# Performance work log

Measured on AMD Instinct MI355X. Metric: run time of the kernel, lower is better.

Reference implementation:

```python
import jax, jax.numpy as jnp
import numpy as np

B, A, C, M, E = 8, 100000, 8, 128, 32
ALPHA, GAMMA = 0.25, 2.0


def setup_inputs() -> dict:
    key = jax.random.key(0)
    k1, k2, k3, k4, k5, k6, k7 = jax.random.split(key, 7)
    classifications = jax.random.uniform(k1, (B, A, C), dtype=jnp.float32)
    regressions = jax.random.normal(k2, (B, A, 8), dtype=jnp.float32)
    embeddings = jax.random.normal(k3, (B, A, E), dtype=jnp.float32)
    # anchors: random centers on a 1920x1080 image, reasonable w/h -> x1,y1,x2,y2
    cx = jax.random.uniform(k4, (A,), minval=0.0, maxval=1920.0)
    cy = jax.random.uniform(jax.random.fold_in(k4, 1), (A,), minval=0.0, maxval=1080.0)
    w = jax.random.uniform(jax.random.fold_in(k4, 2), (A,), minval=16.0, maxval=256.0)
    h = jax.random.uniform(jax.random.fold_in(k4, 3), (A,), minval=16.0, maxval=256.0)
    anchors = jnp.stack([cx - 0.5 * w, cy - 0.5 * h, cx + 0.5 * w, cy + 0.5 * h], axis=1)[None].astype(jnp.float32)
    # annotations: 16 coords = jittered 3D-box corner projections around a random box,
    # col 16 = object id, col 17 = class label in [0, C)
    bcx = jax.random.uniform(k5, (B, M, 1), minval=100.0, maxval=1820.0)
    bcy = jax.random.uniform(jax.random.fold_in(k5, 1), (B, M, 1), minval=100.0, maxval=980.0)
    bw = jax.random.uniform(jax.random.fold_in(k5, 2), (B, M, 1), minval=30.0, maxval=300.0)
    bh = jax.random.uniform(jax.random.fold_in(k5, 3), (B, M, 1), minval=30.0, maxval=300.0)
    jit = jax.random.uniform(k6, (B, M, 16), minval=-0.4, maxval=0.4)
    sx = jnp.array([-1, -1, 1, 1, -1, -1, 1, 1], jnp.float32)
    sy = jnp.array([-1, 1, -1, 1, -1, 1, -1, 1], jnp.float32)
    xs = bcx + 0.5 * bw * (sx + jit[..., 0:16:2])
    ys = bcy + 0.5 * bh * (sy + jit[..., 1:16:2])
    coords = jnp.stack([xs, ys], axis=-1).reshape(B, M, 16)
    ids = jax.random.randint(k7, (B, M, 1), 0, 1000).astype(jnp.float32)
    cls_lab = jax.random.randint(jax.random.fold_in(k7, 1), (B, M, 1), 0, C).astype(jnp.float32)
    annotations = jnp.concatenate([coords, ids, cls_lab], axis=-1)
    return {
        "classifications": classifications,
        "regressions": regressions,
        "anchors": anchors,
        "annotations": annotations,
        "embeddings": embeddings,
    }


def calc_iou(a, b):
    # a: [A,4], b: [M,4] in x1,y1,x2,y2 -> [A,M]
    area = (b[:, 2] - b[:, 0]) * (b[:, 3] - b[:, 1])
    iw = jnp.minimum(a[:, 2:3], b[None, :, 2]) - jnp.maximum(a[:, 0:1], b[None, :, 0])
    ih = jnp.minimum(a[:, 3:4], b[None, :, 3]) - jnp.maximum(a[:, 1:2], b[None, :, 1])
    iw = jnp.clip(iw, 0.0)
    ih = jnp.clip(ih, 0.0)
    ua = ((a[:, 2] - a[:, 0]) * (a[:, 3] - a[:, 1]))[:, None] + area[None, :] - iw * ih
    return iw * ih / jnp.clip(ua, 1e-8)


_S2 = jnp.array([-1, -1, 1, 1, -1, -1, 1, 1], jnp.float32)
_S4 = jnp.array([-1, 1, -1, 1, -1, 1, -1, 1], jnp.float32)
_S6 = jnp.array([1, 1, 1, 1, -1, -1, -1, -1], jnp.float32)


def _per_image(cls, reg, ann, anchor):
    # cls [A,C], reg [A,8], ann [M,18], anchor [A,4]
    aw = anchor[:, 2] - anchor[:, 0]
    ah = anchor[:, 3] - anchor[:, 1]
    acx = anchor[:, 0] + 0.5 * aw
    acy = anchor[:, 1] + 0.5 * ah
    cls = jnp.clip(cls, 1e-4, 1.0 - 1e-4)
    valid = ann[:, -1] >= 0.0  # [M]; annotations with class -1 are padding
    xs, ys = ann[:, 0:16:2], ann[:, 1:16:2]
    box2d = jnp.stack([xs.min(1), ys.min(1), xs.max(1), ys.max(1)], axis=1)  # [M,4]
    iou = jnp.where(valid[None, :], calc_iou(anchor, box2d), -1.0)  # [A,M]
    iou_max = iou.max(1)
    assigned = ann[iou.argmax(1)]  # [A,18]
    pos = iou_max >= 0.5
    neg = iou_max < 0.4
    num_pos = jnp.maximum(pos.sum().astype(cls.dtype), 1.0)

    onehot = jax.nn.one_hot(assigned[:, -1].astype(jnp.int32), cls.shape[1], dtype=cls.dtype)
    targets = jnp.where(pos[:, None], onehot, jnp.where(neg[:, None], 0.0, -1.0))
    alpha_f = jnp.where(targets == 1.0, ALPHA, 1.0 - ALPHA)
    focal_w = alpha_f * jnp.where(targets == 1.0, 1.0 - cls, cls) ** GAMMA
    bce = -(targets * jnp.log(cls) + (1.0 - targets) * jnp.log(1.0 - cls))
    cls_loss = jnp.where(targets != -1.0, focal_w * bce, 0.0).sum() / num_pos

    t = assigned[:, :16]

    def vp(rx, ry, tx, ty):
        denom = jnp.sqrt(rx * rx + ry * ry) * jnp.sqrt(tx * tx + ty * ty)
        return 1.0 - (rx * tx + ry * ty) / jnp.maximum(denom, 1e-8)

    vp1 = vp(reg[:, 2], reg[:, 3],
             (t[:, 4] + t[:, 6] + t[:, 12] + t[:, 14] - (t[:, 0] + t[:, 2] + t[:, 8] + t[:, 10])) / 4.0,
             (t[:, 5] + t[:, 7] + t[:, 13] + t[:, 15] - (t[:, 1] + t[:, 3] + t[:, 9] + t[:, 11])) / 4.0)
    vp2 = vp(reg[:, 4], reg[:, 5],
             (t[:, 2] + t[:, 6] + t[:, 10] + t[:, 14] - (t[:, 0] + t[:, 4] + t[:, 8] + t[:, 12])) / 4.0,
             (t[:, 3] + t[:, 7] + t[:, 11] + t[:, 15] - (t[:, 1] + t[:, 5] + t[:, 9] + t[:, 13])) / 4.0)
    vp3 = vp(reg[:, 6], reg[:, 7],
             (t[:, 0] + t[:, 2] + t[:, 4] + t[:, 6] - (t[:, 8] + t[:, 10] + t[:, 12] + t[:, 14])) / 4.0,
             (t[:, 1] + t[:, 3] + t[:, 5] + t[:, 7] - (t[:, 9] + t[:, 11] + t[:, 13] + t[:, 15])) / 4.0)
    vp_all = (vp1 + vp2 + vp3) / 3.0
    vp_loss = (vp_all * pos).sum() / num_pos

    # corner predictions from (ctr_x, ctr_y, v1, v2, v3) offsets: [A,8] x-coords, [A,8] y-coords
    px = reg[:, 0:1] + reg[:, 2:3] * _S2 + reg[:, 4:5] * _S4 + reg[:, 6:7] * _S6
    py = reg[:, 1:2] + reg[:, 3:4] * _S2 + reg[:, 5:6] * _S4 + reg[:, 7:8] * _S6
    tx = (t[:, 0:16:2] - acx[:, None]) / aw[:, None]
    ty = (t[:, 1:16:2] - acy[:, None]) / ah[:, None]
    diff = jnp.concatenate([jnp.abs(px - tx), jnp.abs(py - ty)], axis=1)  # [A,16]
    sl1 = jnp.where(diff <= 1.0 / 9.0, 0.5 * 9.0 * diff * diff, diff - 0.5 / 9.0)
    reg_loss = (sl1.mean(1) * pos).sum() / num_pos
    return cls_loss, reg_loss, vp_loss


def reference(classifications, regressions, anchors, annotations, embeddings):
    anchor = anchors[0]
    cls_l, reg_l, vp_l = jax.vmap(_per_image, in_axes=(0, 0, 0, None))(
        classifications, regressions, annotations, anchor)
    return jnp.stack([cls_l.mean(), reg_l.mean(), vp_l.mean()])


if __name__ == "__main__":
    print(reference(**setup_inputs()))
```

## Files before the change

### kernel.cpp

```cpp
#include <hip/hip_runtime.h>
#include <hip/hip_bf16.h>

namespace {

constexpr int B_N = 8;
constexpr int A_N = 100000;
constexpr int C_N = 8;
constexpr int M_N = 128;
constexpr int BLOCK = 256;
constexpr int NBLK = (A_N + BLOCK - 1) / BLOCK;

__global__ __launch_bounds__(BLOCK) void focal_main(
    const float* __restrict__ cls_,
    const float* __restrict__ reg_,
    const float* __restrict__ anchors_,
    const float* __restrict__ ann_,
    float* __restrict__ partials)
{
    __shared__ float  s_ann[M_N * 18];
    __shared__ float4 s_bb[M_N];
    __shared__ float4 s_meta[M_N];

    const int b   = blockIdx.y;
    const int tid = threadIdx.x;

    const float* annb = ann_ + (size_t)b * M_N * 18;
    for (int i = tid; i < M_N * 18; i += BLOCK) s_ann[i] = annb[i];
    __syncthreads();
    if (tid < M_N) {
        const float* t = s_ann + tid * 18;
        float minx = t[0], maxx = t[0], miny = t[1], maxy = t[1];
#pragma unroll
        for (int j = 1; j < 8; ++j) {
            minx = fminf(minx, t[2 * j]);     maxx = fmaxf(maxx, t[2 * j]);
            miny = fminf(miny, t[2 * j + 1]); maxy = fmaxf(maxy, t[2 * j + 1]);
        }
        s_bb[tid] = make_float4(minx, miny, maxx, maxy);
        const float area = (maxx - minx) * (maxy - miny);
        const float c    = t[17];
        s_meta[tid] = make_float4(area, c, (c >= 0.0f) ? 1.0f : 0.0f, 0.0f);
    }
    __syncthreads();

    const int a = blockIdx.x * BLOCK + tid;
    float clsS = 0.f, regS = 0.f, vpS = 0.f, posC = 0.f;

    if (a < A_N) {
        const float4 an   = ((const float4*)anchors_)[a];
        const float  aw   = an.z - an.x;
        const float  ah   = an.w - an.y;
        const float  acx  = an.x + 0.5f * aw;
        const float  acy  = an.y + 0.5f * ah;
        const float  aarea = aw * ah;

        float bn = -1.0f, bd = 1.0f;
        int   kbest = 0;
        for (int m = 0; m < M_N; ++m) {
            const float4 bb = s_bb[m];
            const float4 mt = s_meta[m];
            float iw = fminf(an.z, bb.z) - fmaxf(an.x, bb.x);
            float ih = fminf(an.w, bb.w) - fmaxf(an.y, bb.y);
            iw = fmaxf(iw, 0.0f);
            ih = fmaxf(ih, 0.0f);
            const float inter = iw * ih;
            const float ua    = fmaxf(aarea + mt.x - inter, 1e-8f);
            const bool  upd   = (mt.z > 0.0f) && (inter * bd > bn * ua);
            if (upd) { bn = inter; bd = ua; kbest = m; }
        }
        const float iou_max = (bn < 0.0f) ? -1.0f : bn / bd;
        const bool  pos = (iou_max >= 0.5f);
        const bool  neg = (iou_max <  0.4f);

        if (pos | neg) {
            const float* cp = cls_ + ((size_t)b * A_N + a) * C_N;
            const float4 c0 = ((const float4*)cp)[0];
            const float4 c1 = ((const float4*)cp)[1];
            const float pv[8] = {c0.x, c0.y, c0.z, c0.w, c1.x, c1.y, c1.z, c1.w};
            const int kc = pos ? (int)s_meta[kbest].y : -1;
            float sneg = 0.f, pkc = 0.5f, negkc = 0.f;
#pragma unroll
            for (int c = 0; c < C_N; ++c) {
                const float pc   = fminf(fmaxf(pv[c], 1e-4f), 1.0f - 1e-4f);
                const float term = 0.75f * pc * pc * (-__logf(1.0f - pc));
                sneg += term;
                if (c == kc) { pkc = pc; negkc = term; }
            }
            clsS = pos ? (sneg - negkc +
                          0.25f * (1.0f - pkc) * (1.0f - pkc) * (-__logf(pkc)))
                       : sneg;
        }

        if (pos) {
            posC = 1.0f;
            const float* rp = reg_ + ((size_t)b * A_N + a) * 8;
            const float4 r0 = ((const float4*)rp)[0];
            const float4 r1 = ((const float4*)rp)[1];
            const float* t  = s_ann + kbest * 18;
            float tt[16];
#pragma unroll
            for (int j = 0; j < 16; ++j) tt[j] = t[j];

            auto vp = [](float rx, float ry, float tx, float ty) {
                const float denom = sqrtf(rx * rx + ry * ry) * sqrtf(tx * tx + ty * ty);
                return 1.0f - (rx * tx + ry * ty) / fmaxf(denom, 1e-8f);
            };
            const float vp1 = vp(r0.z, r0.w,
                (tt[4] + tt[6] + tt[12] + tt[14] - (tt[0] + tt[2] + tt[8] + tt[10])) * 0.25f,
                (tt[5] + tt[7] + tt[13] + tt[15] - (tt[1] + tt[3] + tt[9] + tt[11])) * 0.25f);
            const float vp2 = vp(r1.x, r1.y,
                (tt[2] + tt[6] + tt[10] + tt[14] - (tt[0] + tt[4] + tt[8] + tt[12])) * 0.25f,
                (tt[3] + tt[7] + tt[11] + tt[15] - (tt[1] + tt[5] + tt[9] + tt[13])) * 0.25f);
            const float vp3 = vp(r1.z, r1.w,
                (tt[0] + tt[2] + tt[4] + tt[6] - (tt[8] + tt[10] + tt[12] + tt[14])) * 0.25f,
                (tt[1] + tt[3] + tt[5] + tt[7] - (tt[9] + tt[11] + tt[13] + tt[15])) * 0.25f);
            vpS = (vp1 + vp2 + vp3) * (1.0f / 3.0f);

            const float s2[8] = {-1, -1, 1, 1, -1, -1, 1, 1};
            const float s4[8] = {-1, 1, -1, 1, -1, 1, -1, 1};
            const float s6[8] = {1, 1, 1, 1, -1, -1, -1, -1};
            float ssum = 0.f;
#pragma unroll
            for (int j = 0; j < 8; ++j) {
                const float px = r0.x + r0.z * s2[j] + r1.x * s4[j] + r1.z * s6[j];
                const float py = r0.y + r0.w * s2[j] + r1.y * s4[j] + r1.w * s6[j];
                const float tx = (tt[2 * j]     - acx) / aw;
                const float ty = (tt[2 * j + 1] - acy) / ah;
                const float dx = fabsf(px - tx);
                const float dy = fabsf(py - ty);
                ssum += (dx <= (1.0f / 9.0f)) ? 4.5f * dx * dx : dx - (0.5f / 9.0f);
                ssum += (dy <= (1.0f / 9.0f)) ? 4.5f * dy * dy : dy - (0.5f / 9.0f);
            }
            regS = ssum * (1.0f / 16.0f);
        }
    }

#pragma unroll
    for (int off = 32; off; off >>= 1) {
        clsS += __shfl_down(clsS, off);
        regS += __shfl_down(regS, off);
        vpS  += __shfl_down(vpS, off);
        posC += __shfl_down(posC, off);
    }
    __shared__ float s_red[4][4];
    const int wv = tid >> 6, ln = tid & 63;
    if (ln == 0) {
        s_red[wv][0] = clsS; s_red[wv][1] = regS;
        s_red[wv][2] = vpS;  s_red[wv][3] = posC;
    }
    __syncthreads();
    if (tid == 0) {
        float C = 0, R = 0, V = 0, P = 0;
        for (int w = 0; w < 4; ++w) {
            C += s_red[w][0]; R += s_red[w][1];
            V += s_red[w][2]; P += s_red[w][3];
        }
        float* out = partials + ((size_t)b * NBLK + blockIdx.x) * 4;
        out[0] = C; out[1] = R; out[2] = V; out[3] = P;
    }
}

__global__ __launch_bounds__(BLOCK) void reduce_img(
    const float* __restrict__ partials,
    float* __restrict__ imgloss)
{
    const int b = blockIdx.x, tid = threadIdx.x;
    float c = 0.f, r = 0.f, v = 0.f, p = 0.f;
    for (int i = tid; i < NBLK; i += BLOCK) {
        const float* q = partials + ((size_t)b * NBLK + i) * 4;
        c += q[0]; r += q[1]; v += q[2]; p += q[3];
    }
#pragma unroll
    for (int off = 32; off; off >>= 1) {
        c += __shfl_down(c, off); r += __shfl_down(r, off);
        v += __shfl_down(v, off); p += __shfl_down(p, off);
    }
    __shared__ float s[4][4];
    const int wv = tid >> 6, ln = tid & 63;
    if (ln == 0) { s[wv][0] = c; s[wv][1] = r; s[wv][2] = v; s[wv][3] = p; }
    __syncthreads();
    if (tid == 0) {
        float C = 0, R = 0, V = 0, P = 0;
        for (int w = 0; w < 4; ++w) {
            C += s[w][0]; R += s[w][1]; V += s[w][2]; P += s[w][3];
        }
        const float np_ = fmaxf(P, 1.0f);
        imgloss[b * 3 + 0] = C / np_;
        imgloss[b * 3 + 1] = R / np_;
        imgloss[b * 3 + 2] = V / np_;
    }
}

__global__ void final_avg(const float* __restrict__ imgloss,
                          float* __restrict__ out)
{
    const int k = threadIdx.x;
    if (k < 3) {
        float s = 0.f;
        for (int b = 0; b < B_N; ++b) s += imgloss[b * 3 + k];
        out[k] = s * 0.125f;
    }
}

}

extern "C" void kernel_launch(void* const* d_in, const int* in_sizes, int n_in,
                              void* d_out, int out_size, void* d_ws, size_t ws_size,
                              hipStream_t stream)
{
    const float* cls_    = (const float*)d_in[0];
    const float* reg_    = (const float*)d_in[1];
    const float* anchors = (const float*)d_in[2];
    const float* ann     = (const float*)d_in[3];

    float* partials = (float*)d_ws;
    float* imgloss  = partials + (size_t)B_N * NBLK * 4;

    dim3 grid(NBLK, B_N);
    focal_main<<<grid, dim3(BLOCK), 0, stream>>>(cls_, reg_, anchors, ann, partials);
    reduce_img<<<dim3(B_N), dim3(BLOCK), 0, stream>>>(partials, imgloss);
    final_avg<<<dim3(1), dim3(64), 0, stream>>>(imgloss, (float*)d_out);
}
```

Before: 78.42 us.

## Process two anchors per thread and streamline the IoU argmax loop

```diff
diff --git a/kernel.cpp b/kernel.cpp
--- a/kernel.cpp
+++ b/kernel.cpp
@@ -8,7 +8,9 @@
 constexpr int C_N = 8;
 constexpr int M_N = 128;
 constexpr int BLOCK = 256;
-constexpr int NBLK = (A_N + BLOCK - 1) / BLOCK;
+constexpr int APT = 2;
+constexpr int TILE = BLOCK * APT;
+constexpr int NBLK = (A_N + TILE - 1) / TILE;
 
 __global__ __launch_bounds__(BLOCK) void focal_main(
     const float* __restrict__ cls_,
@@ -17,88 +19,114 @@
     const float* __restrict__ ann_,
     float* __restrict__ partials)
 {
-    __shared__ float  s_ann[M_N * 18];
     __shared__ float4 s_bb[M_N];
-    __shared__ float4 s_meta[M_N];
+    __shared__ float  s_area[M_N];
 
     const int b   = blockIdx.y;
     const int tid = threadIdx.x;
-
     const float* annb = ann_ + (size_t)b * M_N * 18;
-    for (int i = tid; i < M_N * 18; i += BLOCK) s_ann[i] = annb[i];
+
+    if (tid < M_N) {
+        const float* t = annb + tid * 18;
+        float minx = t[0], maxx = t[0], miny = t[1], maxy = t[1];
+#pragma unroll
+        for (int j = 1; j < 8; ++j) {
+            const float xj = t[2 * j], yj = t[2 * j + 1];
+            minx = fminf(minx, xj); maxx = fmaxf(maxx, xj);
+            miny = fminf(miny, yj); maxy = fmaxf(maxy, yj);
+        }
+        float area = (maxx - minx) * (maxy - miny);
+        if (t[17] < 0.0f) {
+            minx = INFINITY; miny = INFINITY; maxx = -INFINITY; maxy = -INFINITY;
+            area = 0.0f;
+        }
+        s_bb[tid]   = make_float4(minx, miny, maxx, maxy);
+        s_area[tid] = area;
+    }
     __syncthreads();
-    if (tid < M_N) {
-        const float* t = s_ann + tid * 18;
-        float minx = t[0], maxx = t[0], miny = t[1], maxy = t[1];
-#pragma unroll
-        for (int j = 1; j < 8; ++j) {
-            minx = fminf(minx, t[2 * j]);     maxx = fmaxf(maxx, t[2 * j]);
-            miny = fminf(miny, t[2 * j + 1]); maxy = fmaxf(maxy, t[2 * j + 1]);
-        }
-        s_bb[tid] = make_float4(minx, miny, maxx, maxy);
-        const float area = (maxx - minx) * (maxy - miny);
-        const float c    = t[17];
-        s_meta[tid] = make_float4(area, c, (c >= 0.0f) ? 1.0f : 0.0f, 0.0f);
-    }
-    __syncthreads();
-
-    const int a = blockIdx.x * BLOCK + tid;
+
+    const int base = blockIdx.x * TILE;
+    const int a0 = base + tid;
+    const int a1 = base + BLOCK + tid;
+    const int c0 = min(a0, A_N - 1);
+    const int c1 = min(a1, A_N - 1);
+
+    const float4 an0 = ((const float4*)anchors_)[c0];
+    const float4 an1 = ((const float4*)anchors_)[c1];
+    const float aarea0 = (an0.z - an0.x) * (an0.w - an0.y);
+    const float aarea1 = (an1.z - an1.x) * (an1.w - an1.y);
+
+    float bn0 = 0.f, bd0 = 1.f, bn1 = 0.f, bd1 = 1.f;
+    int   kb0 = 0,   kb1 = 0;
+
+#pragma unroll 4
+    for (int m = 0; m < M_N; ++m) {
+        const float4 bb = s_bb[m];
+        const float  ba = s_area[m];
+
+        const float iw0 = fminf(an0.z, bb.z) - fmaxf(an0.x, bb.x);
+        const float ih0 = fminf(an0.w, bb.w) - fmaxf(an0.y, bb.y);
+        const float in0 = fmaxf(iw0, 0.f) * fmaxf(ih0, 0.f);
+        const float ua0 = (aarea0 + ba) - in0;
+        const bool  u0  = in0 * bd0 > bn0 * ua0;
+        bn0 = u0 ? in0 : bn0;
+        bd0 = u0 ? ua0 : bd0;
+        kb0 = u0 ? m   : kb0;
+
+        const float iw1 = fminf(an1.z, bb.z) - fmaxf(an1.x, bb.x);
+        const float ih1 = fminf(an1.w, bb.w) - fmaxf(an1.y, bb.y);
+        const float in1 = fmaxf(iw1, 0.f) * fmaxf(ih1, 0.f);
+        const float ua1 = (aarea1 + ba) - in1;
+        const bool  u1  = in1 * bd1 > bn1 * ua1;
+        bn1 = u1 ? in1 : bn1;
+        bd1 = u1 ? ua1 : bd1;
+        kb1 = u1 ? m   : kb1;
+    }
+
     float clsS = 0.f, regS = 0.f, vpS = 0.f, posC = 0.f;
 
-    if (a < A_N) {
-        const float4 an   = ((const float4*)anchors_)[a];
-        const float  aw   = an.z - an.x;
-        const float  ah   = an.w - an.y;
-        const float  acx  = an.x + 0.5f * aw;
-        const float  acy  = an.y + 0.5f * ah;
-        const float  aarea = aw * ah;
-
-        float bn = -1.0f, bd = 1.0f;
-        int   kbest = 0;
-        for (int m = 0; m < M_N; ++m) {
-            const float4 bb = s_bb[m];
-            const float4 mt = s_meta[m];
-            float iw = fminf(an.z, bb.z) - fmaxf(an.x, bb.x);
-            float ih = fminf(an.w, bb.w) - fmaxf(an.y, bb.y);
-            iw = fmaxf(iw, 0.0f);
-            ih = fmaxf(ih, 0.0f);
-            const float inter = iw * ih;
-            const float ua    = fmaxf(aarea + mt.x - inter, 1e-8f);
-            const bool  upd   = (mt.z > 0.0f) && (inter * bd > bn * ua);
-            if (upd) { bn = inter; bd = ua; kbest = m; }
-        }
-        const float iou_max = (bn < 0.0f) ? -1.0f : bn / bd;
-        const bool  pos = (iou_max >= 0.5f);
-        const bool  neg = (iou_max <  0.4f);
-
-        if (pos | neg) {
-            const float* cp = cls_ + ((size_t)b * A_N + a) * C_N;
-            const float4 c0 = ((const float4*)cp)[0];
-            const float4 c1 = ((const float4*)cp)[1];
-            const float pv[8] = {c0.x, c0.y, c0.z, c0.w, c1.x, c1.y, c1.z, c1.w};
-            const int kc = pos ? (int)s_meta[kbest].y : -1;
-            float sneg = 0.f, pkc = 0.5f, negkc = 0.f;
-#pragma unroll
-            for (int c = 0; c < C_N; ++c) {
-                const float pc   = fminf(fmaxf(pv[c], 1e-4f), 1.0f - 1e-4f);
-                const float term = 0.75f * pc * pc * (-__logf(1.0f - pc));
-                sneg += term;
-                if (c == kc) { pkc = pc; negkc = term; }
-            }
-            clsS = pos ? (sneg - negkc +
-                          0.25f * (1.0f - pkc) * (1.0f - pkc) * (-__logf(pkc)))
-                       : sneg;
-        }
-
+    auto epilogue = [&](int a, const float4& an, float bn, float bd, int kb) {
+        if (a >= A_N) return;
+        const bool pos = (bn + bn) >= bd;
+        const bool neg = (5.0f * bn) < (bd + bd);
+
+        const float* cp = cls_ + ((size_t)b * A_N + a) * C_N;
+        const float4 cA = ((const float4*)cp)[0];
+        const float4 cB = ((const float4*)cp)[1];
+        const float pv[8] = {cA.x, cA.y, cA.z, cA.w, cB.x, cB.y, cB.z, cB.w};
+
+        float tt[16];
+        int   kc = -1;
         if (pos) {
-            posC = 1.0f;
+            const float* t = annb + kb * 18;
+#pragma unroll
+            for (int j = 0; j < 16; ++j) tt[j] = t[j];
+            kc = (int)t[17];
+        }
+
+        float sneg = 0.f, pkc = 0.5f, negkc = 0.f;
+#pragma unroll
+        for (int c = 0; c < C_N; ++c) {
+            const float pc   = fminf(fmaxf(pv[c], 1e-4f), 1.0f - 1e-4f);
+            const float term = 0.75f * pc * pc * (-__logf(1.0f - pc));
+            sneg += term;
+            if (c == kc) { pkc = pc; negkc = term; }
+        }
+        if (pos | neg)
+            clsS += pos ? (sneg - negkc +
+                           0.25f * (1.0f - pkc) * (1.0f - pkc) * (-__logf(pkc)))
+                        : sneg;
+
+        if (pos) {
+            posC += 1.0f;
+            const float aw  = an.z - an.x;
+            const float ah  = an.w - an.y;
+            const float acx = an.x + 0.5f * aw;
+            const float acy = an.y + 0.5f * ah;
+
             const float* rp = reg_ + ((size_t)b * A_N + a) * 8;
             const float4 r0 = ((const float4*)rp)[0];
             const float4 r1 = ((const float4*)rp)[1];
-            const float* t  = s_ann + kbest * 18;
-            float tt[16];
-#pragma unroll
-            for (int j = 0; j < 16; ++j) tt[j] = t[j];
 
             auto vp = [](float rx, float ry, float tx, float ty) {
                 const float denom = sqrtf(rx * rx + ry * ry) * sqrtf(tx * tx + ty * ty);
@@ -113,7 +141,7 @@
             const float vp3 = vp(r1.z, r1.w,
                 (tt[0] + tt[2] + tt[4] + tt[6] - (tt[8] + tt[10] + tt[12] + tt[14])) * 0.25f,
                 (tt[1] + tt[3] + tt[5] + tt[7] - (tt[9] + tt[11] + tt[13] + tt[15])) * 0.25f);
-            vpS = (vp1 + vp2 + vp3) * (1.0f / 3.0f);
+            vpS += (vp1 + vp2 + vp3) * (1.0f / 3.0f);
 
             const float s2[8] = {-1, -1, 1, 1, -1, -1, 1, 1};
             const float s4[8] = {-1, 1, -1, 1, -1, 1, -1, 1};
@@ -130,9 +158,12 @@
                 ssum += (dx <= (1.0f / 9.0f)) ? 4.5f * dx * dx : dx - (0.5f / 9.0f);
                 ssum += (dy <= (1.0f / 9.0f)) ? 4.5f * dy * dy : dy - (0.5f / 9.0f);
             }
-            regS = ssum * (1.0f / 16.0f);
-        }
-    }
+            regS += ssum * (1.0f / 16.0f);
+        }
+    };
+
+    epilogue(a0, an0, bn0, bd0, kb0);
+    epilogue(a1, an1, bn1, bd1, kb1);
 
 #pragma unroll
     for (int off = 32; off; off >>= 1) {
```

Result: slower. 83.76 us (+6.8%).
